# Optimization experiments

Measured on AMD Instinct MI355X. Metric: run time of the kernel, lower is better.

## Reference

```python
import jax, jax.numpy as jnp
import numpy as np


def _lsa_numpy(cost):
    """O(n^3) Jonker-Volgenant / Hungarian (shortest augmenting path with
    potentials). Returns col[i] = column assigned to row i. Matches
    scipy.optimize.linear_sum_assignment for square cost matrices."""
    n = cost.shape[0]
    u = np.zeros(n + 1)
    v = np.zeros(n + 1)
    p = np.zeros(n + 1, dtype=np.int64)   # p[j] = row matched to column j (1-based)
    way = np.zeros(n + 1, dtype=np.int64)
    for i in range(1, n + 1):
        p[0] = i
        j0 = 0
        minv = np.full(n + 1, np.inf)
        used = np.zeros(n + 1, dtype=bool)
        while True:
            used[j0] = True
            i0 = p[j0]
            free = ~used
            free[0] = False
            cur = cost[i0 - 1] - u[i0] - v[1:]
            better = free[1:] & (cur < minv[1:])
            minv[1:] = np.where(better, cur, minv[1:])
            way[1:] = np.where(better, j0, way[1:])
            masked = np.where(free[1:], minv[1:], np.inf)
            j1 = int(np.argmin(masked)) + 1
            delta = masked[j1 - 1]
            u[p[used]] += delta
            v[used] -= delta
            minv[1:] = np.where(free[1:], minv[1:] - delta, minv[1:])
            j0 = j1
            if p[j0] == 0:
                break
        while j0 != 0:
            j1 = int(way[j0])
            p[j0] = p[j1]
            j0 = j1
    col = np.zeros(n, dtype=np.int64)
    for j in range(1, n + 1):
        col[p[j] - 1] = j - 1
    return col


def _batched_lsa(costs):
    costs = np.asarray(costs, dtype=np.float64)
    return np.stack([_lsa_numpy(c) for c in costs]).astype(np.int32)


def _pairwise_dist(pred, target):
    # (B,L,1,D) - (B,1,L,D) -> L2 norm over D, matching torch.norm(x-y, dim=-1)
    return jnp.linalg.norm(pred[:, :, None, :] - target[:, None, :, :], axis=-1)


def setup_inputs() -> dict:
    key = jax.random.key(0)
    k1, k2 = jax.random.split(key)
    B, L, D = 16, 256, 128
    pred = jax.random.normal(k1, (B, L, D), dtype=jnp.float32)
    target = jax.random.normal(k2, (B, L, D), dtype=jnp.float32)
    return {"pred": pred, "target": target}


def reference(pred, target):
    B, L, _ = pred.shape
    dist = _pairwise_dist(pred, target)  # (B, L, L)
    # Hungarian assignment on the detached cost matrices (host callback, like
    # the original's .detach().cpu().numpy() + scipy linear_sum_assignment).
    cols = jax.pure_callback(
        _batched_lsa,
        jax.ShapeDtypeStruct((B, L), jnp.int32),
        jax.lax.stop_gradient(dist),
    )
    # dist[b, r, cols[b, r]] for all rows; reduction='mean' per batch, summed
    # then divided by B == global mean over all matched pairs.
    matched = jnp.take_along_axis(dist, cols[:, :, None], axis=2)[..., 0]  # (B, L)
    return jnp.mean(matched)
```

## Files before the change

kernel.cpp:

```cpp
#include <hip/hip_runtime.h>
#include <hip/hip_fp16.h>
#include <hip/hip_bf16.h>
#include <float.h>
#include <limits.h>

#define B_SZ 16
#define L_SZ 256
#define D_SZ 128

__global__ __launch_bounds__(256) void dist_kernel(const float* __restrict__ pred,
                                                   const float* __restrict__ target,
                                                   float* __restrict__ dist) {
    __shared__ float predRows[8][D_SZ];
    const int blk = blockIdx.x;
    const int b   = blk >> 5;
    const int i0  = (blk & 31) * 8;
    const int tid = threadIdx.x;

    for (int idx = tid; idx < 8 * D_SZ; idx += 256) {
        int r = idx >> 7, d = idx & (D_SZ - 1);
        predRows[r][d] = pred[((size_t)b * L_SZ + i0 + r) * D_SZ + d];
    }
    __syncthreads();

    const int j = tid;
    const float* tr = target + ((size_t)b * L_SZ + j) * D_SZ;
    float acc[8];
#pragma unroll
    for (int r = 0; r < 8; ++r) acc[r] = 0.0f;

    for (int d = 0; d < D_SZ; d += 4) {
        float4 tv = *(const float4*)(tr + d);
#pragma unroll
        for (int r = 0; r < 8; ++r) {
            float4 pv = *(const float4*)(&predRows[r][d]);
            float dx = pv.x - tv.x; acc[r] += dx * dx;
            float dy = pv.y - tv.y; acc[r] += dy * dy;
            float dz = pv.z - tv.z; acc[r] += dz * dz;
            float dw = pv.w - tv.w; acc[r] += dw * dw;
        }
    }
#pragma unroll
    for (int r = 0; r < 8; ++r)
        dist[((size_t)b * L_SZ + i0 + r) * L_SZ + j] = sqrtf(acc[r]);
}

__device__ inline int readlane_i(int x, int l) { return __builtin_amdgcn_readlane(x, l); }
__device__ inline unsigned uminu(unsigned a, unsigned b) { return a < b ? a : b; }
template <int CTRL>
__device__ inline unsigned dpp_mov(unsigned v) {
    return (unsigned)__builtin_amdgcn_update_dpp((int)v, (int)v, CTRL, 0xF, 0xF, false);
}
__device__ inline unsigned wave_umin_bcast(unsigned v) {
    unsigned a = dpp_mov<0x111>(v);
    unsigned b = dpp_mov<0x112>(v);
    v = uminu(uminu(v, a), b);
    a = dpp_mov<0x113>(v);
    b = dpp_mov<0x116>(v);
    v = uminu(uminu(v, a), b);
    a = dpp_mov<0x119>(v);
    v = uminu(v, a);
    a = dpp_mov<0x142>(v);
    v = uminu(v, a);
    a = dpp_mov<0x143>(v);
    v = uminu(v, a);
    return (unsigned)__builtin_amdgcn_readlane((int)v, 63);
}
__device__ inline void unpack4(uint2 pk, float& a, float& b, float& c, float& d) {
    union { unsigned u; __half2 h; } x, y; x.u = pk.x; y.u = pk.y;
    a = __low2float(x.h); b = __high2float(x.h);
    c = __low2float(y.h); d = __high2float(y.h);
}
#define SEL4(a0,a1,a2,a3,k) ((k)==0?(a0):(k)==1?(a1):(k)==2?(a2):(a3))

#define OFF_U      (L_SZ * L_SZ * 2)
#define OFF_CLAIM  (OFF_U + (L_SZ + 1) * 4)
#define OFF_FL     (OFF_CLAIM + (L_SZ + 1) * 4)
#define LSA_LDS_BYTES (OFF_FL + (L_SZ + 1) * 4 + 4)

__global__ __launch_bounds__(64) void lsa_kernel(const float* __restrict__ dist,
                                                 double* __restrict__ partial) {
    extern __shared__ char smem[];
    float* u_lds   = (float*)(smem + OFF_U);
    int*   claimed = (int*)(smem + OFF_CLAIM);
    int*   fl      = (int*)(smem + OFF_FL);

    const int b = blockIdx.x;
    const int t = threadIdx.x;
    const float* cost = dist + (size_t)b * L_SZ * L_SZ;
    const int c0i = 4 * t, c1i = 4 * t + 1, c2i = 4 * t + 2, c3i = 4 * t + 3;

    for (int idx = t * 4; idx < L_SZ * L_SZ; idx += 256) {
        float4 f = *(const float4*)(cost + idx);
        union { unsigned u; __half2 h; } a, c;
        a.h = __floats2half2_rn(f.x, f.y);
        c.h = __floats2half2_rn(f.z, f.w);
        uint2 pk; pk.x = a.u; pk.y = c.u;
        *(uint2*)(smem + idx * 2) = pk;
    }
    __syncthreads();

    float bv0 = FLT_MAX, bv1 = FLT_MAX, bv2 = FLT_MAX, bv3 = FLT_MAX;
    int   br0 = 0, br1 = 0, br2 = 0, br3 = 0;
    for (int i = 1; i <= L_SZ; ++i) {
        uint2 cpk = *(const uint2*)(smem + (size_t)(i - 1) * (L_SZ * 2) + t * 8);
        float c0, c1, c2, c3; unpack4(cpk, c0, c1, c2, c3);
        if (c0 < bv0) { bv0 = c0; br0 = i; }
        if (c1 < bv1) { bv1 = c1; br1 = i; }
        if (c2 < bv2) { bv2 = c2; br2 = i; }
        if (c3 < bv3) { bv3 = c3; br3 = i; }
    }
    float v0 = bv0, v1 = bv1, v2 = bv2, v3 = bv3;

    for (int r = t; r <= L_SZ; r += 64) claimed[r] = INT_MAX;
    __syncthreads();
    atomicMin(&claimed[br0], c0i);
    atomicMin(&claimed[br1], c1i);
    atomicMin(&claimed[br2], c2i);
    atomicMin(&claimed[br3], c3i);
    __syncthreads();
    int p0 = (claimed[br0] == c0i) ? br0 : 0;
    int p1 = (claimed[br1] == c1i) ? br1 : 0;
    int p2 = (claimed[br2] == c2i) ? br2 : 0;
    int p3 = (claimed[br3] == c3i) ? br3 : 0;

    int nf = 0;
    for (int blk = 0; blk < 4; ++blk) {
        int r = blk * 64 + t + 1;
        bool isfree = (claimed[r] == INT_MAX);
        unsigned long long mask = __ballot(isfree);
        int before = __popcll(mask & ((1ULL << t) - 1ULL));
        if (isfree) fl[nf + before] = r;
        nf += (int)__popcll(mask);
    }
    __syncthreads();

    int numfree = nf;
    int budget = 1024;
    for (int pass = 0; pass < 2; ++pass) {
        int kq = 0, prv = numfree; numfree = 0;
        while (kq < prv && budget > 0) {
            budget--;
            int i = fl[kq]; kq++;
            uint2 cpk = *(const uint2*)(smem + (size_t)(i - 1) * (L_SZ * 2) + t * 8);
            float cc0, cc1, cc2, cc3; unpack4(cpk, cc0, cc1, cc2, cc3);
            float rc0 = cc0 - v0, rc1 = cc1 - v1, rc2 = cc2 - v2, rc3 = cc3 - v3;
            float m1 = rc0; int j1 = c0i; float m2 = FLT_MAX; int j2 = INT_MAX;
            if (rc1 < m1) { m2 = m1; j2 = j1; m1 = rc1; j1 = c1i; } else if (rc1 < m2) { m2 = rc1; j2 = c1i; }
            if (rc2 < m1) { m2 = m1; j2 = j1; m1 = rc2; j1 = c2i; } else if (rc2 < m2) { m2 = rc2; j2 = c2i; }
            if (rc3 < m1) { m2 = m1; j2 = j1; m1 = rc3; j1 = c3i; } else if (rc3 < m2) { m2 = rc3; j2 = c3i; }
#pragma unroll
            for (int off = 1; off < 64; off <<= 1) {
                float bm1 = __shfl_xor(m1, off, 64); int bj1 = __shfl_xor(j1, off, 64);
                float bm2 = __shfl_xor(m2, off, 64); int bj2 = __shfl_xor(j2, off, 64);
                bool bw = (bm1 < m1) || (bm1 == m1 && bj1 < j1);
                if (bw) {
                    if (bm2 < m1 || (bm2 == m1 && bj2 < j1)) { m2 = bm2; j2 = bj2; }
                    else { m2 = m1; j2 = j1; }
                    m1 = bm1; j1 = bj1;
                } else {
                    if (bm1 < m2 || (bm1 == m2 && bj1 < j2)) { m2 = bm1; j2 = bj1; }
                }
            }
            int t1 = j1 >> 2, k1 = j1 & 3;
            int i0 = readlane_i(SEL4(p0, p1, p2, p3, k1), t1);
            bool strict = (m1 < m2);
            int jt, i0t;
            if (strict) {
                jt = j1; i0t = i0;
                float amt = m2 - m1;
                if (t == t1) {
                    if (k1 == 0) v0 -= amt; else if (k1 == 1) v1 -= amt;
                    else if (k1 == 2) v2 -= amt; else v3 -= amt;
                }
            } else if (i0 != 0) {
                jt = j2; i0t = readlane_i(SEL4(p0, p1, p2, p3, j2 & 3), j2 >> 2);
            } else { jt = j1; i0t = 0; }
            {
                int tt = jt >> 2, kk = jt & 3;
                if (t == tt) {
                    if (kk == 0) p0 = i; else if (kk == 1) p1 = i;
                    else if (kk == 2) p2 = i; else p3 = i;
                }
            }
            if (i0t != 0) {
                if (strict) { kq--; if (t == 0) fl[kq] = i0t; }
                else        { if (t == 0) fl[numfree] = i0t; numfree++; }
            }
            __syncthreads();
        }
        if (budget <= 0) break;
    }

    __syncthreads();
    for (int r = t; r <= L_SZ; r += 64) { claimed[r] = 0; u_lds[r] = 0.0f; }
    __syncthreads();
    if (p0) claimed[p0] = 1;
    if (p1) claimed[p1] = 1;
    if (p2) claimed[p2] = 1;
    if (p3) claimed[p3] = 1;
    __syncthreads();
    int nfree = 0;
    for (int blk = 0; blk < 4; ++blk) {
        int r = blk * 64 + t + 1;
        bool isfree = (claimed[r] == 0);
        unsigned long long mask = __ballot(isfree);
        int before = __popcll(mask & ((1ULL << t) - 1ULL));
        if (isfree) fl[nfree + before] = r;
        nfree += (int)__popcll(mask);
    }
    __syncthreads();
    const __half* ch = (const __half*)smem;
    if (p0) u_lds[p0] = __half2float(ch[(size_t)(p0 - 1) * L_SZ + c0i]) - v0;
    if (p1) u_lds[p1] = __half2float(ch[(size_t)(p1 - 1) * L_SZ + c1i]) - v1;
    if (p2) u_lds[p2] = __half2float(ch[(size_t)(p2 - 1) * L_SZ + c2i]) - v2;
    if (p3) u_lds[p3] = __half2float(ch[(size_t)(p3 - 1) * L_SZ + c3i]) - v3;
    __syncthreads();

    const unsigned HB  = __float_as_uint(1e30f) & 0xFFFFFF00u;
    const unsigned hp0 = HB | (unsigned)c0i, hp1 = HB | (unsigned)c1i;
    const unsigned hp2 = HB | (unsigned)c2i, hp3 = HB | (unsigned)c3i;
    float vsh0 = v0, vsh1 = v1, vsh2 = v2, vsh3 = v3;

    for (int f = 0; f < nfree; ++f) {
        const int icur = fl[f];
        unsigned s0 = 0x7F7FFF00u | (unsigned)c0i;
        unsigned s1 = 0x7F7FFF00u | (unsigned)c1i;
        unsigned s2 = 0x7F7FFF00u | (unsigned)c2i;
        unsigned s3 = 0x7F7FFF00u | (unsigned)c3i;
        int w0 = -1, w1 = -1, w2 = -1, w3 = -1;
        float ds0 = 0.f, ds1 = 0.f, ds2 = 0.f, ds3 = 0.f;
        float dj0 = 0.f;
        int   j0  = -1;
        int jS = 0; float dfin = 0.f;

        uint2 cur = *(const uint2*)(smem + (size_t)(icur - 1) * (L_SZ * 2) + t * 8);
        float ui0 = u_lds[icur];

        for (int it = 0; it <= L_SZ; ++it) {
            float cc0, cc1, cc2, cc3; unpack4(cur, cc0, cc1, cc2, cc3);
            const float base = dj0 - ui0;
            float n0 = fmaxf((cc0 - vsh0) + base, 0.0f);
            float n1 = fmaxf((cc1 - vsh1) + base, 0.0f);
            float n2 = fmaxf((cc2 - vsh2) + base, 0.0f);
            float n3 = fmaxf((cc3 - vsh3) + base, 0.0f);
            unsigned np0 = (__float_as_uint(n0) & 0xFFFFFF00u) | (unsigned)c0i;
            unsigned np1 = (__float_as_uint(n1) & 0xFFFFFF00u) | (unsigned)c1i;
            unsigned np2 = (__float_as_uint(n2) & 0xFFFFFF00u) | (unsigned)c2i;
            unsigned np3 = (__float_as_uint(n3) & 0xFFFFFF00u) | (unsigned)c3i;
            bool b0 = np0 < s0, b1 = np1 < s1, b2 = np2 < s2, b3 = np3 < s3;
            w0 = b0 ? j0 : w0;  s0 = b0 ? np0 : s0;
            w1 = b1 ? j0 : w1;  s1 = b1 ? np1 : s1;
            w2 = b2 ? j0 : w2;  s2 = b2 ? np2 : s2;
            w3 = b3 ? j0 : w3;  s3 = b3 ? np3 : s3;

            unsigned m01 = uminu(s0, s1), m23 = uminu(s2, s3);
            unsigned m4  = uminu(m01, m23);
            int kloc = (int)(m4 & 3u);
            int myi  = SEL4(p0, p1, p2, p3, kloc);

            const unsigned pk = wave_umin_bcast(m4);
            const int   j1    = (int)(pk & 255u);
            const int   t1    = j1 >> 2;
            const float delta = __uint_as_float(pk & 0xFFFFFF00u);
            const int   i1    = readlane_i(myi, t1);

            if (i1 == 0 || it == L_SZ) { jS = j1; dfin = delta; break; }

            bool e0 = (c0i == j1), e1 = (c1i == j1), e2 = (c2i == j1), e3 = (c3i == j1);
            vsh0 = e0 ? -1e30f : vsh0;  s0 = e0 ? hp0 : s0;  ds0 = e0 ? delta : ds0;
            vsh1 = e1 ? -1e30f : vsh1;  s1 = e1 ? hp1 : s1;  ds1 = e1 ? delta : ds1;
            vsh2 = e2 ? -1e30f : vsh2;  s2 = e2 ? hp2 : s2;  ds2 = e2 ? delta : ds2;
            vsh3 = e3 ? -1e30f : vsh3;  s3 = e3 ? hp3 : s3;  ds3 = e3 ? delta : ds3;

            cur = *(const uint2*)(smem + (size_t)(i1 - 1) * (L_SZ * 2) + t * 8);
            ui0 = u_lds[i1];

            j0 = j1; dj0 = delta;
        }

        if (vsh0 < -1e29f) { u_lds[p0] += dfin - ds0; v0 += ds0 - dfin; }
        if (vsh1 < -1e29f) { u_lds[p1] += dfin - ds1; v1 += ds1 - dfin; }
        if (vsh2 < -1e29f) { u_lds[p2] += dfin - ds2; v2 += ds2 - dfin; }
        if (vsh3 < -1e29f) { u_lds[p3] += dfin - ds3; v3 += ds3 - dfin; }
        if (t == 0) u_lds[icur] += dfin;
        vsh0 = v0; vsh1 = v1; vsh2 = v2; vsh3 = v3;
        __syncthreads();

        int j = jS;
        for (int st = 0; st <= L_SZ; ++st) {
            int tj = j >> 2, kj = j & 3;
            int jn = readlane_i(SEL4(w0, w1, w2, w3, kj), tj);
            int pn;
            if (jn < 0) pn = icur;
            else pn = readlane_i(SEL4(p0, p1, p2, p3, jn & 3), jn >> 2);
            if (t == tj) {
                if (kj == 0) p0 = pn; else if (kj == 1) p1 = pn;
                else if (kj == 2) p2 = pn; else p3 = pn;
            }
            if (jn < 0) break;
            j = jn;
        }
    }

    double s = 0.0;
    s += (double)cost[(size_t)max(p0 - 1, 0) * L_SZ + c0i];
    s += (double)cost[(size_t)max(p1 - 1, 0) * L_SZ + c1i];
    s += (double)cost[(size_t)max(p2 - 1, 0) * L_SZ + c2i];
    s += (double)cost[(size_t)max(p3 - 1, 0) * L_SZ + c3i];
#pragma unroll
    for (int off = 1; off < 64; off <<= 1) s += __shfl_xor(s, off, 64);
    if (t == 0) partial[b] = s;
}

__global__ void finalize_kernel(const double* __restrict__ partial, float* __restrict__ out) {
    double s = 0.0;
    for (int b = 0; b < B_SZ; ++b) s += partial[b];
    out[0] = (float)(s / (double)(B_SZ * L_SZ));
}

extern "C" void kernel_launch(void* const* d_in, const int* in_sizes, int n_in,
                              void* d_out, int out_size, void* d_ws, size_t ws_size,
                              hipStream_t stream) {
    const float* pred   = (const float*)d_in[0];
    const float* target = (const float*)d_in[1];
    float* out = (float*)d_out;

    float*  dist    = (float*)d_ws;
    double* partial = (double*)((char*)d_ws + (size_t)B_SZ * L_SZ * L_SZ * sizeof(float));

    (void)hipFuncSetAttribute((const void*)lsa_kernel,
                              hipFuncAttributeMaxDynamicSharedMemorySize,
                              LSA_LDS_BYTES);

    dist_kernel<<<B_SZ * L_SZ / 8, 256, 0, stream>>>(pred, target, dist);
    lsa_kernel<<<B_SZ, 64, LSA_LDS_BYTES, stream>>>(dist, partial);
    finalize_kernel<<<1, 1, 0, stream>>>(partial, out);
}
```

Measured before the change: 2.212 ms.

## Augment multiple free rows per Dijkstra phase with multi-source shortest paths

Replaces the one-free-row-at-a-time Hungarian augmentation with phased multi-source Dijkstra. All free rows seed the search at once, the scan runs until up to nfr free columns are reached, and then vertex-disjoint augmenting paths are applied, with use-bitmasks checked per lane. The goal is fewer total Dijkstra scans and fewer potential updates per free row during the final cleanup stage. The cost is a longer scan per phase, extra serial path tracing, and a possible loss of optimality or extra phases, since dual updates use a single dfin for every root.

```diff
diff --git a/kernel.cpp b/kernel.cpp
--- a/kernel.cpp
+++ b/kernel.cpp
@@ -76,7 +76,8 @@
 #define OFF_U      (L_SZ * L_SZ * 2)
 #define OFF_CLAIM  (OFF_U + (L_SZ + 1) * 4)
 #define OFF_FL     (OFF_CLAIM + (L_SZ + 1) * 4)
-#define LSA_LDS_BYTES (OFF_FL + (L_SZ + 1) * 4 + 4)
+#define OFF_EP     (OFF_FL + (L_SZ + 1) * 4)
+#define LSA_LDS_BYTES (OFF_EP + L_SZ * 4 + 4)
 
 __global__ __launch_bounds__(64) void lsa_kernel(const float* __restrict__ dist,
                                                  double* __restrict__ partial) {
@@ -84,6 +85,7 @@
     float* u_lds   = (float*)(smem + OFF_U);
     int*   claimed = (int*)(smem + OFF_CLAIM);
     int*   fl      = (int*)(smem + OFF_FL);
+    int*   ep      = (int*)(smem + OFF_EP);
 
     const int b = blockIdx.x;
     const int t = threadIdx.x;
@@ -193,22 +195,7 @@
     }
 
     __syncthreads();
-    for (int r = t; r <= L_SZ; r += 64) { claimed[r] = 0; u_lds[r] = 0.0f; }
-    __syncthreads();
-    if (p0) claimed[p0] = 1;
-    if (p1) claimed[p1] = 1;
-    if (p2) claimed[p2] = 1;
-    if (p3) claimed[p3] = 1;
-    __syncthreads();
-    int nfree = 0;
-    for (int blk = 0; blk < 4; ++blk) {
-        int r = blk * 64 + t + 1;
-        bool isfree = (claimed[r] == 0);
-        unsigned long long mask = __ballot(isfree);
-        int before = __popcll(mask & ((1ULL << t) - 1ULL));
-        if (isfree) fl[nfree + before] = r;
-        nfree += (int)__popcll(mask);
-    }
+    for (int r = t; r <= L_SZ; r += 64) u_lds[r] = 0.0f;
     __syncthreads();
     const __half* ch = (const __half*)smem;
     if (p0) u_lds[p0] = __half2float(ch[(size_t)(p0 - 1) * L_SZ + c0i]) - v0;
@@ -222,24 +209,87 @@
     const unsigned hp2 = HB | (unsigned)c2i, hp3 = HB | (unsigned)c3i;
     float vsh0 = v0, vsh1 = v1, vsh2 = v2, vsh3 = v3;
 
-    for (int f = 0; f < nfree; ++f) {
-        const int icur = fl[f];
+    for (int phase = 0; phase < 300; ++phase) {
+        for (int r = t; r <= L_SZ; r += 64) claimed[r] = 0;
+        __syncthreads();
+        if (p0) claimed[p0] = 1;
+        if (p1) claimed[p1] = 1;
+        if (p2) claimed[p2] = 1;
+        if (p3) claimed[p3] = 1;
+        __syncthreads();
+        int nfr = 0;
+        for (int blk = 0; blk < 4; ++blk) {
+            int r = blk * 64 + t + 1;
+            bool isfree = (claimed[r] == 0);
+            unsigned long long mask = __ballot(isfree);
+            int before = __popcll(mask & ((1ULL << t) - 1ULL));
+            if (isfree) fl[nfr + before] = r;
+            nfr += (int)__popcll(mask);
+        }
+        __syncthreads();
+        if (nfr == 0) break;
+
         unsigned s0 = 0x7F7FFF00u | (unsigned)c0i;
         unsigned s1 = 0x7F7FFF00u | (unsigned)c1i;
         unsigned s2 = 0x7F7FFF00u | (unsigned)c2i;
         unsigned s3 = 0x7F7FFF00u | (unsigned)c3i;
         int w0 = -1, w1 = -1, w2 = -1, w3 = -1;
         float ds0 = 0.f, ds1 = 0.f, ds2 = 0.f, ds3 = 0.f;
-        float dj0 = 0.f;
-        int   j0  = -1;
-        int jS = 0; float dfin = 0.f;
-
-        uint2 cur = *(const uint2*)(smem + (size_t)(icur - 1) * (L_SZ * 2) + t * 8);
-        float ui0 = u_lds[icur];
-
-        for (int it = 0; it <= L_SZ; ++it) {
+        int cu = 0, ru = 0;
+
+        for (int k = 0; k < nfr; ++k) {
+            int fr = fl[k];
+            uint2 cr = *(const uint2*)(smem + (size_t)(fr - 1) * (L_SZ * 2) + t * 8);
+            float ufr = u_lds[fr];
+            float cc0, cc1, cc2, cc3; unpack4(cr, cc0, cc1, cc2, cc3);
+            float n0 = fmaxf((cc0 - vsh0) - ufr, 0.0f);
+            float n1 = fmaxf((cc1 - vsh1) - ufr, 0.0f);
+            float n2 = fmaxf((cc2 - vsh2) - ufr, 0.0f);
+            float n3 = fmaxf((cc3 - vsh3) - ufr, 0.0f);
+            unsigned np0 = (__float_as_uint(n0) & 0xFFFFFF00u) | (unsigned)c0i;
+            unsigned np1 = (__float_as_uint(n1) & 0xFFFFFF00u) | (unsigned)c1i;
+            unsigned np2 = (__float_as_uint(n2) & 0xFFFFFF00u) | (unsigned)c2i;
+            unsigned np3 = (__float_as_uint(n3) & 0xFFFFFF00u) | (unsigned)c3i;
+            int src = -(fr + 1);
+            bool b0 = np0 < s0, b1 = np1 < s1, b2 = np2 < s2, b3 = np3 < s3;
+            w0 = b0 ? src : w0;  s0 = b0 ? np0 : s0;
+            w1 = b1 ? src : w1;  s1 = b1 ? np1 : s1;
+            w2 = b2 ? src : w2;  s2 = b2 ? np2 : s2;
+            w3 = b3 ? src : w3;  s3 = b3 ? np3 : s3;
+        }
+
+        int found = 0;
+        float dfin = 0.f;
+        for (int it = 0; it < 2 * L_SZ + 4; ++it) {
+            unsigned m01 = uminu(s0, s1), m23 = uminu(s2, s3);
+            unsigned m4  = uminu(m01, m23);
+            int kloc = (int)(m4 & 3u);
+            int myi  = SEL4(p0, p1, p2, p3, kloc);
+
+            const unsigned pk = wave_umin_bcast(m4);
+            const int   j1    = (int)(pk & 255u);
+            const int   t1    = j1 >> 2;
+            const float delta = __uint_as_float(pk & 0xFFFFFF00u);
+            const int   i1    = readlane_i(myi, t1);
+            dfin = delta;
+
+            bool e0 = (c0i == j1), e1 = (c1i == j1), e2 = (c2i == j1), e3 = (c3i == j1);
+            vsh0 = e0 ? -1e30f : vsh0;  s0 = e0 ? hp0 : s0;  ds0 = e0 ? delta : ds0;
+            vsh1 = e1 ? -1e30f : vsh1;  s1 = e1 ? hp1 : s1;  ds1 = e1 ? delta : ds1;
+            vsh2 = e2 ? -1e30f : vsh2;  s2 = e2 ? hp2 : s2;  ds2 = e2 ? delta : ds2;
+            vsh3 = e3 ? -1e30f : vsh3;  s3 = e3 ? hp3 : s3;  ds3 = e3 ? delta : ds3;
+
+            if (i1 == 0) {
+                if (t == 0) ep[found] = j1;
+                found++;
+                if (found == nfr) break;
+                continue;
+            }
+
+            uint2 cur = *(const uint2*)(smem + (size_t)(i1 - 1) * (L_SZ * 2) + t * 8);
+            float ui = u_lds[i1];
             float cc0, cc1, cc2, cc3; unpack4(cur, cc0, cc1, cc2, cc3);
-            const float base = dj0 - ui0;
+            const float base = delta - ui;
             float n0 = fmaxf((cc0 - vsh0) + base, 0.0f);
             float n1 = fmaxf((cc1 - vsh1) + base, 0.0f);
             float n2 = fmaxf((cc2 - vsh2) + base, 0.0f);
@@ -249,57 +299,56 @@
             unsigned np2 = (__float_as_uint(n2) & 0xFFFFFF00u) | (unsigned)c2i;
             unsigned np3 = (__float_as_uint(n3) & 0xFFFFFF00u) | (unsigned)c3i;
             bool b0 = np0 < s0, b1 = np1 < s1, b2 = np2 < s2, b3 = np3 < s3;
-            w0 = b0 ? j0 : w0;  s0 = b0 ? np0 : s0;
-            w1 = b1 ? j0 : w1;  s1 = b1 ? np1 : s1;
-            w2 = b2 ? j0 : w2;  s2 = b2 ? np2 : s2;
-            w3 = b3 ? j0 : w3;  s3 = b3 ? np3 : s3;
-
-            unsigned m01 = uminu(s0, s1), m23 = uminu(s2, s3);
-            unsigned m4  = uminu(m01, m23);
-            int kloc = (int)(m4 & 3u);
-            int myi  = SEL4(p0, p1, p2, p3, kloc);
-
-            const unsigned pk = wave_umin_bcast(m4);
-            const int   j1    = (int)(pk & 255u);
-            const int   t1    = j1 >> 2;
-            const float delta = __uint_as_float(pk & 0xFFFFFF00u);
-            const int   i1    = readlane_i(myi, t1);
-
-            if (i1 == 0 || it == L_SZ) { jS = j1; dfin = delta; break; }
-
-            bool e0 = (c0i == j1), e1 = (c1i == j1), e2 = (c2i == j1), e3 = (c3i == j1);
-            vsh0 = e0 ? -1e30f : vsh0;  s0 = e0 ? hp0 : s0;  ds0 = e0 ? delta : ds0;
-            vsh1 = e1 ? -1e30f : vsh1;  s1 = e1 ? hp1 : s1;  ds1 = e1 ? delta : ds1;
-            vsh2 = e2 ? -1e30f : vsh2;  s2 = e2 ? hp2 : s2;  ds2 = e2 ? delta : ds2;
-            vsh3 = e3 ? -1e30f : vsh3;  s3 = e3 ? hp3 : s3;  ds3 = e3 ? delta : ds3;
-
-            cur = *(const uint2*)(smem + (size_t)(i1 - 1) * (L_SZ * 2) + t * 8);
-            ui0 = u_lds[i1];
-
-            j0 = j1; dj0 = delta;
-        }
+            w0 = b0 ? j1 : w0;  s0 = b0 ? np0 : s0;
+            w1 = b1 ? j1 : w1;  s1 = b1 ? np1 : s1;
+            w2 = b2 ? j1 : w2;  s2 = b2 ? np2 : s2;
+            w3 = b3 ? j1 : w3;  s3 = b3 ? np3 : s3;
+        }
+        __syncthreads();
 
         if (vsh0 < -1e29f) { u_lds[p0] += dfin - ds0; v0 += ds0 - dfin; }
         if (vsh1 < -1e29f) { u_lds[p1] += dfin - ds1; v1 += ds1 - dfin; }
         if (vsh2 < -1e29f) { u_lds[p2] += dfin - ds2; v2 += ds2 - dfin; }
         if (vsh3 < -1e29f) { u_lds[p3] += dfin - ds3; v3 += ds3 - dfin; }
-        if (t == 0) u_lds[icur] += dfin;
+        for (int k = t; k < nfr; k += 64) u_lds[fl[k]] += dfin;
         vsh0 = v0; vsh1 = v1; vsh2 = v2; vsh3 = v3;
         __syncthreads();
 
-        int j = jS;
-        for (int st = 0; st <= L_SZ; ++st) {
-            int tj = j >> 2, kj = j & 3;
-            int jn = readlane_i(SEL4(w0, w1, w2, w3, kj), tj);
-            int pn;
-            if (jn < 0) pn = icur;
-            else pn = readlane_i(SEL4(p0, p1, p2, p3, jn & 3), jn >> 2);
-            if (t == tj) {
-                if (kj == 0) p0 = pn; else if (kj == 1) p1 = pn;
-                else if (kj == 2) p2 = pn; else p3 = pn;
-            }
-            if (jn < 0) break;
-            j = jn;
+        for (int k = 0; k < found; ++k) {
+            int je = ep[k];
+            int j = je, root = -1; bool ok = true;
+            for (int st = 0; st <= L_SZ; ++st) {
+                int tj = j >> 2, kj = j & 3;
+                int usebits = readlane_i(cu, tj);
+                if ((usebits >> kj) & 1) { ok = false; break; }
+                int wj = readlane_i(SEL4(w0, w1, w2, w3, kj), tj);
+                if (wj < 0) {
+                    root = -wj - 1;
+                    int rl = (root - 1) >> 2, rb = (root - 1) & 3;
+                    int rbits = readlane_i(ru, rl);
+                    ok = !((rbits >> rb) & 1);
+                    break;
+                }
+                j = wj;
+            }
+            if (!ok || root < 1) continue;
+            j = je;
+            for (int st = 0; st <= L_SZ; ++st) {
+                int tj = j >> 2, kj = j & 3;
+                int wj = readlane_i(SEL4(w0, w1, w2, w3, kj), tj);
+                int wsafe = wj < 0 ? 0 : wj;
+                int pn = (wj < 0) ? root
+                        : readlane_i(SEL4(p0, p1, p2, p3, wsafe & 3), wsafe >> 2);
+                if (t == tj) {
+                    if (kj == 0) p0 = pn; else if (kj == 1) p1 = pn;
+                    else if (kj == 2) p2 = pn; else p3 = pn;
+                    cu |= (1 << kj);
+                }
+                if (wj < 0) break;
+                j = wj;
+            }
+            int rl = (root - 1) >> 2, rb = (root - 1) & 3;
+            if (t == rl) ru |= (1 << rb);
         }
     }
 
```

Measured after the change: 2.570 ms. 16.2% more time.
